# Performance work log

Measured on AMD Instinct MI355X. Metric: run time of the kernel, lower is better.

Reference implementation:

```python
import jax, jax.numpy as jnp
import numpy as np


def _sign(x):
    # sign(r) = 1 if r > 0 else -1 (matches 2*(r>0)-1 in the torch code)
    return 2.0 * (x > 0).astype(x.dtype) - 1.0


def setup_inputs() -> dict:
    key = jax.random.key(0)
    k1, k2 = jax.random.split(key)
    x = jax.random.normal(k1, (32, 256, 56, 56), dtype=jnp.float32)
    weight = jax.random.normal(k2, (256, 256, 3, 3), dtype=jnp.float32)
    alpha = jnp.ones((256, 1, 1), dtype=jnp.float32)
    return {"x": x, "weight": weight, "alpha": alpha}


def reference(x, weight, alpha):
    # conv2d(sign(x), sign(W), stride=1, padding=1) * alpha
    out = jax.lax.conv_general_dilated(
        _sign(x), _sign(weight),
        window_strides=(1, 1),
        padding=[(1, 1), (1, 1)],
        dimension_numbers=("NCHW", "OIHW", "NCHW"),
    )
    return out * alpha  # alpha: (C_out, 1, 1) broadcasts over (N, C_out, H, W)
```

## Files before the change

### kernel.cpp

```cpp
#include <hip/hip_runtime.h>
#include <stdint.h>

typedef unsigned long long u64;

#define CIN    256
#define COUT   256
#define HW     56
#define NPIX   (HW * HW)
#define PADW   58
#define PPIX   (PADW * PADW)
#define NBATCH 32

__global__ __launch_bounds__(256) void pack_x_kernel(const float* __restrict__ x,
                                                     u64* __restrict__ xb) {
    int g   = blockIdx.x * 256 + threadIdx.x;
    int wq  = g & 3;
    int rem = g >> 2;
    int p   = rem % NPIX;
    int n   = rem / NPIX;
    const float* xp = x + ((size_t)(n * CIN + wq * 64)) * NPIX + p;
    u64 word = 0;
#pragma unroll
    for (int j = 0; j < 64; ++j) {
        word |= (u64)(xp[(size_t)j * NPIX] > 0.0f) << j;
    }
    int h = p / HW, w = p % HW;
    xb[((size_t)n * PPIX + (size_t)(h + 1) * PADW + (w + 1)) * 4 + wq] = word;
}

__global__ __launch_bounds__(256) void pack_w_kernel(const float* __restrict__ wt,
                                                     u64* __restrict__ wb) {
    int g = blockIdx.x * 256 + threadIdx.x;
    if (g >= COUT * 9) return;
    int co = g / 9, k = g % 9;
#pragma unroll
    for (int q = 0; q < 4; ++q) {
        u64 word = 0;
#pragma unroll
        for (int j = 0; j < 64; ++j) {
            float v = wt[((size_t)(co * CIN + q * 64 + j)) * 9 + k];
            word |= (u64)(v > 0.0f) << j;
        }
        wb[((size_t)co * 9 + k) * 4 + q] = word;
    }
}

__global__ __launch_bounds__(256) void make_ab_kernel(const u64* __restrict__ wb,
                                                      const float* __restrict__ alpha,
                                                      float* __restrict__ A,
                                                      float* __restrict__ B) {
    int co = blockIdx.x * 256 + threadIdx.x;
    if (co >= COUT) return;
    int kpop[9];
#pragma unroll
    for (int k = 0; k < 9; ++k) {
        int s = 0;
#pragma unroll
        for (int q = 0; q < 4; ++q) s += __popcll(wb[((size_t)co * 9 + k) * 4 + q]);
        kpop[k] = s;
    }
    float al = alpha[co];
    B[co] = 2.0f * al;
#pragma unroll
    for (int cls = 0; cls < 9; ++cls) {
        int ch = cls / 3, cw = cls % 3;
        int wcl = 0, vcnt = 0;
#pragma unroll
        for (int k = 0; k < 9; ++k) {
            int kh = k / 3, kw = k % 3;
            bool inv = (kh == 0 && ch == 0) || (kh == 2 && ch == 2) ||
                       (kw == 0 && cw == 0) || (kw == 2 && cw == 2);
            if (inv) wcl += kpop[k]; else vcnt++;
        }
        A[co * 9 + cls] = al * (float)(256 * vcnt + 2 * wcl);
    }
}

__global__ __launch_bounds__(256) void conv_kernel(const u64* __restrict__ xb,
                                                   const u64* __restrict__ wb,
                                                   const float* __restrict__ A,
                                                   const float* __restrict__ B,
                                                   float* __restrict__ out) {
    int tid   = threadIdx.x;
    int ptile = blockIdx.x;
    int n     = blockIdx.y;
    int chunk = blockIdx.z;
    int p = ptile * 256 + tid;
    if (p >= NPIX) return;
    int h = p / HW, w = p % HW;

    u64 xn[9][4];
    const u64* xbase = xb + ((size_t)n * PPIX + (size_t)h * PADW + w) * 4;
#pragma unroll
    for (int dh = 0; dh < 3; ++dh)
#pragma unroll
        for (int dw = 0; dw < 3; ++dw)
#pragma unroll
            for (int q = 0; q < 4; ++q)
                xn[dh * 3 + dw][q] = xbase[((size_t)dh * PADW + dw) * 4 + q];

    int ch  = (h == 0) ? 0 : ((h == HW - 1) ? 2 : 1);
    int cw  = (w == 0) ? 0 : ((w == HW - 1) ? 2 : 1);
    int cls = ch * 3 + cw;

    int co0 = chunk * 64;
    const u64*   wp = wb + (size_t)co0 * 36;
    float*       op = out + ((size_t)(n * COUT + co0)) * NPIX + p;
    const float* Ap = A + co0 * 9 + cls;
    const float* Bp = B + co0;

    for (int c = 0; c < 64; ++c) {
        int acc0 = 0, acc1 = 0;
#pragma unroll
        for (int k = 0; k < 9; ++k) {
#pragma unroll
            for (int q = 0; q < 4; ++q) {
                int pc = __popcll(xn[k][q] ^ wp[k * 4 + q]);
                if ((k ^ q) & 1) acc1 += pc; else acc0 += pc;
            }
        }
        op[0] = Ap[c * 9] - Bp[c] * (float)(acc0 + acc1);
        op += NPIX;
        wp += 36;
    }
}

extern "C" void kernel_launch(void* const* d_in, const int* in_sizes, int n_in,
                              void* d_out, int out_size, void* d_ws, size_t ws_size,
                              hipStream_t stream) {
    const float* x     = (const float*)d_in[0];
    const float* wt    = (const float*)d_in[1];
    const float* alpha = (const float*)d_in[2];
    float* out = (float*)d_out;

    char* ws = (char*)d_ws;
    u64* xb = (u64*)ws;
    size_t xb_bytes = (size_t)NBATCH * PPIX * 4 * sizeof(u64);
    u64* wb = (u64*)(ws + xb_bytes);
    size_t wb_bytes = (size_t)COUT * 9 * 4 * sizeof(u64);
    float* A = (float*)(ws + xb_bytes + wb_bytes);
    float* B = A + COUT * 9;

    hipMemsetAsync(xb, 0, xb_bytes, stream);

    pack_x_kernel<<<dim3(NBATCH * NPIX * 4 / 256), 256, 0, stream>>>(x, xb);
    pack_w_kernel<<<dim3(9), 256, 0, stream>>>(wt, wb);
    make_ab_kernel<<<dim3(1), 256, 0, stream>>>(wb, alpha, A, B);
    conv_kernel<<<dim3(13, NBATCH, 4), 256, 0, stream>>>(xb, wb, A, B, out);
}
```

Baseline: 327.0 us.

## Coalesce x packing, fuse weight packing via ballot, tweak conv accumulators

```diff
diff --git a/kernel.cpp b/kernel.cpp
--- a/kernel.cpp
+++ b/kernel.cpp
@@ -13,57 +13,46 @@
 
 __global__ __launch_bounds__(256) void pack_x_kernel(const float* __restrict__ x,
                                                      u64* __restrict__ xb) {
-    int g   = blockIdx.x * 256 + threadIdx.x;
-    int wq  = g & 3;
-    int rem = g >> 2;
-    int p   = rem % NPIX;
-    int n   = rem / NPIX;
-    const float* xp = x + ((size_t)(n * CIN + wq * 64)) * NPIX + p;
+    int p = blockIdx.x * 256 + threadIdx.x;
+    int n = blockIdx.y;
+    int q = blockIdx.z;
+    if (p >= NPIX) return;
+    const float* xp = x + ((size_t)(n * CIN + q * 64)) * NPIX + p;
     u64 word = 0;
 #pragma unroll
     for (int j = 0; j < 64; ++j) {
         word |= (u64)(xp[(size_t)j * NPIX] > 0.0f) << j;
     }
     int h = p / HW, w = p % HW;
-    xb[((size_t)n * PPIX + (size_t)(h + 1) * PADW + (w + 1)) * 4 + wq] = word;
+    xb[((size_t)n * PPIX + (size_t)(h + 1) * PADW + (w + 1)) * 4 + q] = word;
 }
 
-__global__ __launch_bounds__(256) void pack_w_kernel(const float* __restrict__ wt,
-                                                     u64* __restrict__ wb) {
-    int g = blockIdx.x * 256 + threadIdx.x;
-    if (g >= COUT * 9) return;
-    int co = g / 9, k = g % 9;
-#pragma unroll
-    for (int q = 0; q < 4; ++q) {
-        u64 word = 0;
-#pragma unroll
-        for (int j = 0; j < 64; ++j) {
-            float v = wt[((size_t)(co * CIN + q * 64 + j)) * 9 + k];
-            word |= (u64)(v > 0.0f) << j;
-        }
-        wb[((size_t)co * 9 + k) * 4 + q] = word;
-    }
-}
-
-__global__ __launch_bounds__(256) void make_ab_kernel(const u64* __restrict__ wb,
+__global__ __launch_bounds__(64) void packw_ab_kernel(const float* __restrict__ wt,
                                                       const float* __restrict__ alpha,
+                                                      u64* __restrict__ wb,
                                                       float* __restrict__ A,
                                                       float* __restrict__ B) {
-    int co = blockIdx.x * 256 + threadIdx.x;
-    if (co >= COUT) return;
+    int co   = blockIdx.x;
+    int lane = threadIdx.x;
+    u64 myword = 0;
     int kpop[9];
 #pragma unroll
     for (int k = 0; k < 9; ++k) {
-        int s = 0;
+        int kp = 0;
 #pragma unroll
-        for (int q = 0; q < 4; ++q) s += __popcll(wb[((size_t)co * 9 + k) * 4 + q]);
-        kpop[k] = s;
+        for (int q = 0; q < 4; ++q) {
+            float v = wt[((size_t)(co * CIN + q * 64 + lane)) * 9 + k];
+            u64 mask = __ballot(v > 0.0f);
+            kp += __popcll(mask);
+            if (lane == k * 4 + q) myword = mask;
+        }
+        kpop[k] = kp;
     }
+    if (lane < 36) wb[(size_t)co * 36 + lane] = myword;
     float al = alpha[co];
-    B[co] = 2.0f * al;
-#pragma unroll
-    for (int cls = 0; cls < 9; ++cls) {
-        int ch = cls / 3, cw = cls % 3;
+    if (lane == 0) B[co] = 2.0f * al;
+    if (lane < 9) {
+        int ch = lane / 3, cw = lane % 3;
         int wcl = 0, vcnt = 0;
 #pragma unroll
         for (int k = 0; k < 9; ++k) {
@@ -72,15 +61,15 @@
                        (kw == 0 && cw == 0) || (kw == 2 && cw == 2);
             if (inv) wcl += kpop[k]; else vcnt++;
         }
-        A[co * 9 + cls] = al * (float)(256 * vcnt + 2 * wcl);
+        A[co * 9 + lane] = al * (float)(256 * vcnt + 2 * wcl);
     }
 }
 
-__global__ __launch_bounds__(256) void conv_kernel(const u64* __restrict__ xb,
-                                                   const u64* __restrict__ wb,
-                                                   const float* __restrict__ A,
-                                                   const float* __restrict__ B,
-                                                   float* __restrict__ out) {
+__global__ __launch_bounds__(256, 4) void conv_kernel(const u64* __restrict__ xb,
+                                                      const u64* __restrict__ wb,
+                                                      const float* __restrict__ A,
+                                                      const float* __restrict__ B,
+                                                      float* __restrict__ out) {
     int tid   = threadIdx.x;
     int ptile = blockIdx.x;
     int n     = blockIdx.y;
@@ -110,16 +99,16 @@
     const float* Bp = B + co0;
 
     for (int c = 0; c < 64; ++c) {
-        int acc0 = 0, acc1 = 0;
+        int acc[4] = {0, 0, 0, 0};
 #pragma unroll
         for (int k = 0; k < 9; ++k) {
 #pragma unroll
             for (int q = 0; q < 4; ++q) {
-                int pc = __popcll(xn[k][q] ^ wp[k * 4 + q]);
-                if ((k ^ q) & 1) acc1 += pc; else acc0 += pc;
+                acc[q] += __popcll(xn[k][q] ^ wp[k * 4 + q]);
             }
         }
-        op[0] = Ap[c * 9] - Bp[c] * (float)(acc0 + acc1);
+        int pc = (acc[0] + acc[1]) + (acc[2] + acc[3]);
+        op[0] = Ap[c * 9] - Bp[c] * (float)pc;
         op += NPIX;
         wp += 36;
     }
@@ -143,8 +132,7 @@
 
     hipMemsetAsync(xb, 0, xb_bytes, stream);
 
-    pack_x_kernel<<<dim3(NBATCH * NPIX * 4 / 256), 256, 0, stream>>>(x, xb);
-    pack_w_kernel<<<dim3(9), 256, 0, stream>>>(wt, wb);
-    make_ab_kernel<<<dim3(1), 256, 0, stream>>>(wb, alpha, A, B);
+    pack_x_kernel<<<dim3(13, NBATCH, 4), 256, 0, stream>>>(x, xb);
+    packw_ab_kernel<<<dim3(COUT), 64, 0, stream>>>(wt, alpha, wb, A, B);
     conv_kernel<<<dim3(13, NBATCH, 4), 256, 0, stream>>>(xb, wb, A, B, out);
 }
```

Measured after the change: 309.6 us. 5.3% less time.
